# Kernel optimization log

Hardware: AMD Instinct MI355X
Metric: run time of the kernel (lower is better)

Reference implementation:

```python
import jax, jax.numpy as jnp
import numpy as np

B, C, E, TARGET = 8, 256, 18000, 4500


def setup_inputs() -> dict:
    key = jax.random.key(0)
    k1, k2 = jax.random.split(key)
    fe = jax.random.normal(k1, (B, C, E), dtype=jnp.float32)
    # group_ids[b, e] = index of the pooled output edge that original edge e
    # was merged into by the union-find during edge collapse.
    group_ids = jax.random.randint(k2, (B, E), 0, TARGET, dtype=jnp.int64)
    return {"fe": fe, "group_ids": group_ids, "target": TARGET}


def reference(fe, group_ids, target):
    # MeshUnion.rebuild_features: out feature of each surviving edge group =
    # mean of features of all original edges merged into that group.
    b, c, e = fe.shape
    # flatten (batch, group) into one segment id so a single segment_sum handles all meshes
    flat_ids = (jnp.arange(b, dtype=group_ids.dtype)[:, None] * target + group_ids).reshape(-1)  # [B*E]
    feats = fe.transpose(0, 2, 1).reshape(b * e, c)  # [B*E, C]
    sums = jax.ops.segment_sum(feats, flat_ids, num_segments=b * target)          # [B*T, C]
    counts = jax.ops.segment_sum(jnp.ones((b * e,), fe.dtype), flat_ids,
                                 num_segments=b * target)                          # [B*T]
    out = sums / jnp.maximum(counts, 1.0)[:, None]
    return out.reshape(b, target, c).transpose(0, 2, 1)  # [B, C, target]
```

## Files before the change

### kernel.cpp

```cpp
#include <hip/hip_runtime.h>

#define BB 8
#define CC 256
#define EE 18000
#define TT 4500
#define BT (BB * TT)
#define BE (BB * EE)
#define NT 512
#define W  36
#define PW (NT * W)


__global__ void zero_counts_kernel(int* __restrict__ counts) {
    int i = blockIdx.x * blockDim.x + threadIdx.x;
    if (i < BT) counts[i] = 0;
}

__global__ void count_kernel(const int* __restrict__ gid, int* __restrict__ counts) {
    int i = blockIdx.x * blockDim.x + threadIdx.x;
    if (i < BE) {
        int b = i / EE;
        atomicAdd(&counts[b * TT + gid[i]], 1);
    }
}

__global__ __launch_bounds__(1024) void scan_kernel(const int* __restrict__ counts,
                                                    int* __restrict__ cursor,
                                                    uint2* __restrict__ tab) {
    __shared__ int part[1024];
    const int b = blockIdx.x;
    const int t = threadIdx.x;
    const int CHUNK = 5;
    int lo = t * CHUNK; if (lo > TT) lo = TT;
    int hi = lo + CHUNK; if (hi > TT) hi = TT;
    int s = 0;
    for (int i = lo; i < hi; ++i) s += counts[b * TT + i];
    part[t] = s;
    __syncthreads();
    for (int d = 1; d < 1024; d <<= 1) {
        int v = (t >= d) ? part[t - d] : 0;
        __syncthreads();
        part[t] += v;
        __syncthreads();
    }
    int run = part[t] - s;
    for (int i = lo; i < hi; ++i) {
        int cnt = counts[b * TT + i];
        cursor[b * TT + i] = b * EE + run;
        int en = run + cnt;
        float inv = cnt ? 1.0f / (float)cnt : 0.0f;
        tab[b * TT + i] = make_uint2((unsigned)run | ((unsigned)en << 16),
                                     __float_as_uint(inv));
        run = en;
    }
}

__global__ void scatter_kernel(const int* __restrict__ gid,
                               int* __restrict__ cursor,
                               unsigned short* __restrict__ prank16) {
    int i = blockIdx.x * blockDim.x + threadIdx.x;
    if (i < BE) {
        int b = i / EE;
        int p = atomicAdd(&cursor[b * TT + gid[i]], 1) - b * EE;
        prank16[i] = (unsigned short)p;
    }
}


__global__ __launch_bounds__(512, 4) void pool_kernel(const float* __restrict__ fe,
                                                      const unsigned short* __restrict__ prank16,
                                                      const uint2* __restrict__ tab,
                                                      float* __restrict__ out) {
    __shared__ float vals[PW];
    __shared__ float wsum[8];
    const int b   = blockIdx.x >> 8;
    const int c   = blockIdx.x & 255;
    const int tid = threadIdx.x;
    const int wv  = tid >> 6;
    const int ln  = tid & 63;

    const float4*  fe4 = (const float4*)(fe + (size_t)(b * CC + c) * EE);
    const ushort4* rk4 = (const ushort4*)(prank16 + (size_t)b * EE);
#pragma unroll
    for (int i = 0; i < 9; ++i) {
        int idx = tid + (i << 9);
        if (idx < EE / 4) {
            float4  v = fe4[idx];
            ushort4 r = rk4[idx];
            vals[r.x] = v.x;
            vals[r.y] = v.y;
            vals[r.z] = v.z;
            vals[r.w] = v.w;
        }
    }
    __syncthreads();

    const int base = W * tid;
    float4 pv[9];
    float  csum[9];
#pragma unroll
    for (int k = 0; k < 9; ++k) {
        float4 v = *reinterpret_cast<float4*>(&vals[base + (k << 2)]);
        float p0 = v.x;
        float p1 = p0 + v.y;
        float p2 = p1 + v.z;
        float p3 = p2 + v.w;
        pv[k] = make_float4(p0, p1, p2, p3);
        csum[k] = p3;
    }
    float t01 = csum[0] + csum[1], t23 = csum[2] + csum[3];
    float t45 = csum[4] + csum[5], t67 = csum[6] + csum[7];
    const float sum = ((t01 + t23) + (t45 + t67)) + csum[8];

    float sc = sum;
#pragma unroll
    for (int d = 1; d < 64; d <<= 1) {
        float o = __shfl_up(sc, d, 64);
        if (ln >= d) sc += o;
    }
    if (ln == 63) wsum[wv] = sc;
    __syncthreads();

    float cross = 0.0f;
#pragma unroll
    for (int j = 0; j < 8; ++j) {
        float tw = wsum[j];
        if (j < wv) cross += tw;
    }

    float off = cross + (sc - sum);
#pragma unroll
    for (int k = 0; k < 9; ++k) {
        float4 p = pv[k];
        float4 o = make_float4(p.x + off, p.y + off, p.z + off, p.w + off);
        *reinterpret_cast<float4*>(&vals[base + (k << 2)]) = o;
        off += csum[k];
    }
    __syncthreads();

    const uint2* tb   = tab + b * TT;
    float*       outb = out + (size_t)(b * CC + c) * TT;
#pragma unroll
    for (int k = 0; k < 9; ++k) {
        int g = tid + (k << 9);
        if (g < TT) {
            uint2 q = tb[g];
            unsigned int st = q.x & 0xffffu;
            unsigned int en = q.x >> 16;
            float Pa = en ? vals[en - 1] : 0.0f;
            float Pb = st ? vals[st - 1] : 0.0f;
            outb[g] = (Pa - Pb) * __uint_as_float(q.y);
        }
    }
}

extern "C" void kernel_launch(void* const* d_in, const int* in_sizes, int n_in,
                              void* d_out, int out_size, void* d_ws, size_t ws_size,
                              hipStream_t stream) {
    const float* fe  = (const float*)d_in[0];
    const int*   gid = (const int*)d_in[1];
    float*       out = (float*)d_out;

    int*            counts  = (int*)d_ws;
    int*            cursor  = counts + BT;
    uint2*          tab     = (uint2*)(cursor + BT);
    unsigned short* prank16 = (unsigned short*)(tab + BT);

    zero_counts_kernel<<<(BT + 255) / 256, 256, 0, stream>>>(counts);
    count_kernel<<<(BE + 255) / 256, 256, 0, stream>>>(gid, counts);
    scan_kernel<<<BB, 1024, 0, stream>>>(counts, cursor, tab);
    scatter_kernel<<<(BE + 255) / 256, 256, 0, stream>>>(gid, cursor, prank16);
    pool_kernel<<<BB * CC, 512, 0, stream>>>(fe, prank16, tab, out);
}
```

Before: 70.31 us.

## Use 1024-thread pool blocks and vectorize output gather over 4 groups

The pool kernel now runs 1024 threads per block, and each thread scans 18 prefix elements instead of 36, which halves the per-thread serial scan work. The output phase handles four consecutive groups per thread: it loads their table entries as two uint4 reads and writes a float4. It reuses each group's end prefix as the next group's start, so it does fewer LDS reads. This relies on groups being contiguous in the prefix array. More waves per block means more cross-wave sync overhead, and shared memory use stays at about 72KB.

Measured after the change: 62.80 us. 1.12x faster.

```diff
diff --git a/kernel.cpp b/kernel.cpp
--- a/kernel.cpp
+++ b/kernel.cpp
@@ -6,8 +6,8 @@
 #define TT 4500
 #define BT (BB * TT)
 #define BE (BB * EE)
-#define NT 512
-#define W  36
+#define NT 1024
+#define W  18
 #define PW (NT * W)
 
 
@@ -67,12 +67,12 @@
 }
 
 
-__global__ __launch_bounds__(512, 4) void pool_kernel(const float* __restrict__ fe,
-                                                      const unsigned short* __restrict__ prank16,
-                                                      const uint2* __restrict__ tab,
-                                                      float* __restrict__ out) {
+__global__ __launch_bounds__(1024, 8) void pool_kernel(const float* __restrict__ fe,
+                                                       const unsigned short* __restrict__ prank16,
+                                                       const uint2* __restrict__ tab,
+                                                       float* __restrict__ out) {
     __shared__ float vals[PW];
-    __shared__ float wsum[8];
+    __shared__ float wsum[16];
     const int b   = blockIdx.x >> 8;
     const int c   = blockIdx.x & 255;
     const int tid = threadIdx.x;
@@ -82,8 +82,8 @@
     const float4*  fe4 = (const float4*)(fe + (size_t)(b * CC + c) * EE);
     const ushort4* rk4 = (const ushort4*)(prank16 + (size_t)b * EE);
 #pragma unroll
-    for (int i = 0; i < 9; ++i) {
-        int idx = tid + (i << 9);
+    for (int i = 0; i < 5; ++i) {
+        int idx = tid + (i << 10);
         if (idx < EE / 4) {
             float4  v = fe4[idx];
             ushort4 r = rk4[idx];
@@ -96,17 +96,15 @@
     __syncthreads();
 
     const int base = W * tid;
-    float4 pv[9];
+    float2 pv[9];
     float  csum[9];
 #pragma unroll
     for (int k = 0; k < 9; ++k) {
-        float4 v = *reinterpret_cast<float4*>(&vals[base + (k << 2)]);
+        float2 v = *reinterpret_cast<const float2*>(&vals[base + (k << 1)]);
         float p0 = v.x;
         float p1 = p0 + v.y;
-        float p2 = p1 + v.z;
-        float p3 = p2 + v.w;
-        pv[k] = make_float4(p0, p1, p2, p3);
-        csum[k] = p3;
+        pv[k] = make_float2(p0, p1);
+        csum[k] = p1;
     }
     float t01 = csum[0] + csum[1], t23 = csum[2] + csum[3];
     float t45 = csum[4] + csum[5], t67 = csum[6] + csum[7];
@@ -123,7 +121,7 @@
 
     float cross = 0.0f;
 #pragma unroll
-    for (int j = 0; j < 8; ++j) {
+    for (int j = 0; j < 16; ++j) {
         float tw = wsum[j];
         if (j < wv) cross += tw;
     }
@@ -131,26 +129,40 @@
     float off = cross + (sc - sum);
 #pragma unroll
     for (int k = 0; k < 9; ++k) {
-        float4 p = pv[k];
-        float4 o = make_float4(p.x + off, p.y + off, p.z + off, p.w + off);
-        *reinterpret_cast<float4*>(&vals[base + (k << 2)]) = o;
+        float2 p = pv[k];
+        *reinterpret_cast<float2*>(&vals[base + (k << 1)]) =
+            make_float2(p.x + off, p.y + off);
         off += csum[k];
     }
     __syncthreads();
 
-    const uint2* tb   = tab + b * TT;
+    const uint2* tbB  = tab + b * TT;
     float*       outb = out + (size_t)(b * CC + c) * TT;
-#pragma unroll
-    for (int k = 0; k < 9; ++k) {
-        int g = tid + (k << 9);
-        if (g < TT) {
-            uint2 q = tb[g];
-            unsigned int st = q.x & 0xffffu;
-            unsigned int en = q.x >> 16;
-            float Pa = en ? vals[en - 1] : 0.0f;
-            float Pb = st ? vals[st - 1] : 0.0f;
-            outb[g] = (Pa - Pb) * __uint_as_float(q.y);
-        }
+    for (int s = tid; s < TT / 4; s += NT) {
+        const uint2* tb = tbB + (s << 2);
+        uint4 qA = *reinterpret_cast<const uint4*>(tb);
+        uint4 qB = *reinterpret_cast<const uint4*>(tb + 2);
+
+        unsigned se0 = qA.x, se1 = qA.z, se2 = qB.x, se3 = qB.z;
+        float iv0 = __uint_as_float(qA.y), iv1 = __uint_as_float(qA.w);
+        float iv2 = __uint_as_float(qB.y), iv3 = __uint_as_float(qB.w);
+
+        unsigned st0 = se0 & 0xffffu;
+        unsigned en0 = se0 >> 16, en1 = se1 >> 16, en2 = se2 >> 16, en3 = se3 >> 16;
+
+        float Pp = vals[(st0 ? st0 : 1u) - 1u]; Pp = st0 ? Pp : 0.0f;
+        float P0 = vals[(en0 ? en0 : 1u) - 1u]; P0 = en0 ? P0 : 0.0f;
+        float P1 = vals[(en1 ? en1 : 1u) - 1u]; P1 = en1 ? P1 : 0.0f;
+        float P2 = vals[(en2 ? en2 : 1u) - 1u]; P2 = en2 ? P2 : 0.0f;
+        float P3 = vals[(en3 ? en3 : 1u) - 1u]; P3 = en3 ? P3 : 0.0f;
+
+        float4 o;
+        o.x = (P0 - Pp) * iv0;
+        o.y = (P1 - P0) * iv1;
+        o.z = (P2 - P1) * iv2;
+        o.w = (P3 - P2) * iv3;
+
+        *reinterpret_cast<float4*>(outb + (s << 2)) = o;
     }
 }
 
@@ -170,5 +182,5 @@
     count_kernel<<<(BE + 255) / 256, 256, 0, stream>>>(gid, counts);
     scan_kernel<<<BB, 1024, 0, stream>>>(counts, cursor, tab);
     scatter_kernel<<<(BE + 255) / 256, 256, 0, stream>>>(gid, cursor, prank16);
-    pool_kernel<<<BB * CC, 512, 0, stream>>>(fe, prank16, tab, out);
+    pool_kernel<<<BB * CC, 1024, 0, stream>>>(fe, prank16, tab, out);
 }
```
